# Optimization experiments

Measured on AMD Instinct MI355X. Metric: run time of the kernel, lower is better.

The kernel has to match this reference:

```python
import jax, jax.numpy as jnp
import numpy as np

EPS_KERNEL = 1e-4
EPS_DENOM = 1e-8


def setup_inputs() -> dict:
    key = jax.random.key(0)
    k1, k2, k3, k4 = jax.random.split(key, 4)
    b, h, n, d = 4, 8, 8192, 64
    nb_features = 266
    return {
        "q": jax.random.normal(k1, (b, h, n, d), dtype=jnp.float32),
        "k": jax.random.normal(k2, (b, h, n, d), dtype=jnp.float32),
        "v": jax.random.normal(k3, (b, h, n, d), dtype=jnp.float32),
        "proj": jax.random.normal(k4, (nb_features, d), dtype=jnp.float32),
    }


def _softmax_kernel(data, proj, is_query):
    # data: [b,h,n,d], proj: [f,d]
    d = data.shape[-1]
    data_normalizer = d ** (-0.25)
    ratio = proj.shape[0] ** (-0.5)
    data_dash = jnp.einsum('bhid,jd->bhij', data_normalizer * data, proj)  # [b,h,n,f]
    diag_data = (jnp.sum(data * data, axis=-1) * 0.5 * data_normalizer ** 2)[..., None]
    if is_query:
        return ratio * (jnp.exp(data_dash - diag_data
                                - jnp.max(data_dash, axis=-1, keepdims=True)) + EPS_KERNEL)
    return ratio * jnp.exp(data_dash - diag_data + EPS_KERNEL)


def reference(q, k, v, proj):
    qp = _softmax_kernel(q, proj, is_query=True)   # [b,h,n,f]
    kp = _softmax_kernel(k, proj, is_query=False)  # [b,h,n,f]
    # non-causal linear attention (never materializes the n x n matrix)
    context = jnp.einsum('bhnf,bhne->bhfe', kp, v)              # [b,h,f,e]
    d_inv = 1.0 / (jnp.einsum('bhnf,bhf->bhn', qp, kp.sum(axis=-2)) + EPS_DENOM)
    return jnp.einsum('bhfe,bhnf,bhn->bhne', context, qp, d_inv)  # [b,h,n,e]
```

## Files before the change

### kernel.cpp

```cpp
#include <hip/hip_runtime.h>
#include <hip/hip_bf16.h>
#include <math.h>


typedef __attribute__((ext_vector_type(8))) short s16x8;
typedef __attribute__((ext_vector_type(4))) float f32x4;

#define MFMA16(a,b,c) __builtin_amdgcn_mfma_f32_16x16x32_bf16((a),(b),(c),0,0,0)

__device__ __forceinline__ unsigned short bf16rne(float x){
  union { __hip_bfloat16 b; unsigned short u; } cv;
  cv.b = __float2bfloat16(x);
  return cv.u;
}
__device__ __forceinline__ float bf16tof(unsigned short h){
  return __uint_as_float(((unsigned)h) << 16);
}
__device__ __forceinline__ float exp2_fast(float x){
#if __has_builtin(__builtin_amdgcn_exp2f)
  return __builtin_amdgcn_exp2f(x);
#else
  float r; asm("v_exp_f32 %0, %1" : "=v"(r) : "v"(x)); return r;
#endif
}
__device__ __forceinline__ void cvt_hl8(const float v[8], s16x8& h, s16x8& l){
  #pragma unroll
  for(int j=0;j<8;++j){
    unsigned short hh = bf16rne(v[j]);
    h[j] = (short)hh;
    l[j] = (short)bf16rne(v[j] - bf16tof(hh));
  }
}

__global__ void fa21_prep(const float* __restrict__ proj, short* __restrict__ ph,
                          float pscale){
  int idx = blockIdx.x*256 + threadIdx.x;
  if(idx >= 288*64) return;
  int f = idx >> 6, dc = idx & 63;
  float v = (f < 266) ? proj[f*64 + dc]*pscale : 0.f;
  ph[idx] = (short)bf16rne(v);
}

__global__ __launch_bounds__(1024,1) void fa21_p1(
    const float* __restrict__ kin, const float* __restrict__ vin,
    const short* __restrict__ pjh,
    float* __restrict__ ctx_part, float* __restrict__ ksum_part,
    float koff, float diagc){
  extern __shared__ char smem[];
  char* sph = smem;
  char* skh = smem + 40960;
  float* ex = (float*)smem;
  const int tid = threadIdx.x;
  const int w = tid >> 6, lane = tid & 63, g = lane >> 4, q = lane & 15;
  const int bid = blockIdx.x;
  const int head = bid & 31, chunk = bid >> 5;
  for(int i = tid; i < 2560; i += 1024){
    int f = i >> 3;
    int byt = (f*128 + (i & 7)*16) ^ ((f & 7) << 4);
    s16x8 vh8 = {0,0,0,0,0,0,0,0};
    if(f < 288) vh8 = ((const s16x8*)pjh)[i];
    *(s16x8*)(sph + byt) = vh8;
  }
  const int mtp = w & 3, fqp = w >> 2;
  const int et  = w & 3, fqc = w >> 2;
  f32x4 acc[5];
  #pragma unroll
  for(int a=0;a<5;++a){ f32x4 z = {0.f,0.f,0.f,0.f}; acc[a] = z; }
  float ksacc[5] = {0.f,0.f,0.f,0.f,0.f};
  const float* kbase = kin + (size_t)head*8192*64;
  const float* vbase = vin + (size_t)head*8192*64;
  const float* xp  = kbase + (size_t)(chunk*1024 + mtp*16 + q)*64 + g*8;
  const float* vp  = vbase + (size_t)(chunk*1024 + 8*g)*64 + et*16 + q;
  const float* vp2 = vp + 2048;
  float4 xa0 = *(const float4*)(xp);
  float4 xb0 = *(const float4*)(xp + 4);
  float4 xa1 = *(const float4*)(xp + 32);
  float4 xb1 = *(const float4*)(xp + 36);
  __syncthreads();
  #pragma unroll 1
  for(int it = 0; it < 16; ++it){
    char* kcur = skh + (it & 1)*40960;
    s16x8 xh[2], xl[2];
    float diag;
    {
      float v0[8] = {xa0.x,xa0.y,xa0.z,xa0.w,xb0.x,xb0.y,xb0.z,xb0.w};
      float v1[8] = {xa1.x,xa1.y,xa1.z,xa1.w,xb1.x,xb1.y,xb1.z,xb1.w};
      float ss = 0.f;
      #pragma unroll
      for(int j=0;j<8;++j){ ss += v0[j]*v0[j]; ss += v1[j]*v1[j]; }
      cvt_hl8(v0, xh[0], xl[0]);
      cvt_hl8(v1, xh[1], xl[1]);
      ss += __shfl_xor(ss, 16); ss += __shfl_xor(ss, 32);
      diag = ss * diagc;
    }
    float dro[4];
    #pragma unroll
    for(int i=0;i<4;++i) dro[i] = __shfl(diag, 4*g + i) - koff;
    s16x8 vh[2], vl[2];
    {
      float vv[8];
      #pragma unroll
      for(int i2=0;i2<8;++i2) vv[i2] = vp[i2*64];
      cvt_hl8(vv, vh[0], vl[0]);
      #pragma unroll
      for(int i2=0;i2<8;++i2) vv[i2] = vp2[i2*64];
      cvt_hl8(vv, vh[1], vl[1]);
    }
    vp += 4096; vp2 += 4096;
    f32x4 S[5];
    #pragma unroll
    for(int t=0;t<5;++t){ f32x4 z = {0.f,0.f,0.f,0.f}; S[t] = z; }
    #pragma unroll
    for(int t=0; t<5; ++t){
      const int gt = fqp*5 + t;
      if(gt > 16) continue;
      const int f = gt*16 + q;
      #pragma unroll
      for(int ks=0; ks<2; ++ks){
        int byt = (f*128 + ks*64 + g*16) ^ ((f & 7) << 4);
        s16x8 bph = *(const s16x8*)(sph + byt);
        S[t] = MFMA16(xh[ks], bph, S[t]);
        S[t] = MFMA16(xl[ks], bph, S[t]);
      }
    }
    #pragma unroll
    for(int t=0; t<5; ++t){
      const int gt = fqp*5 + t;
      if(gt > 16) continue;
      const int f = gt*16 + q;
      float p[4];
      #pragma unroll
      for(int i=0;i<4;++i) p[i] = exp2_fast(S[t][i] - dro[i]);
      if(gt == 16){
        #pragma unroll
        for(int i=0;i<4;++i) p[i] = (q < 10) ? p[i] : 0.f;
      }
      ksacc[t] += p[0]+p[1]+p[2]+p[3];
      uint2 hv;
      hv.x = (unsigned)bf16rne(p[0]) | ((unsigned)bf16rne(p[1]) << 16);
      hv.y = (unsigned)bf16rne(p[2]) | ((unsigned)bf16rne(p[3]) << 16);
      int byt = (f*128 + (mtp*16 + 4*g)*2) ^ ((f & 7) << 4);
      *(uint2*)(kcur + byt) = hv;
    }
    xp += 4096;
    if(it < 15){
      xa0 = *(const float4*)(xp);
      xb0 = *(const float4*)(xp + 4);
      xa1 = *(const float4*)(xp + 32);
      xb1 = *(const float4*)(xp + 36);
    }
    __syncthreads();
    #pragma unroll
    for(int fm=0; fm<5; ++fm){
      const int gt = fqc*5 + fm;
      if(gt > 16) continue;
      const int fg = gt*16 + q;
      #pragma unroll
      for(int ks=0; ks<2; ++ks){
        int byt = (fg*128 + ks*64 + g*16) ^ ((fg & 7) << 4);
        s16x8 kf = *(const s16x8*)(kcur + byt);
        acc[fm] = MFMA16(kf, vh[ks], acc[fm]);
        acc[fm] = MFMA16(kf, vl[ks], acc[fm]);
      }
    }
  }
  {
    float* cp = ctx_part + (size_t)bid*288*64;
    #pragma unroll
    for(int fm=0; fm<5; ++fm){
      const int gt = fqc*5 + fm;
      if(gt < 18){
        #pragma unroll
        for(int i=0;i<4;++i){
          int f = gt*16 + 4*g + i;
          cp[f*64 + et*16 + q] = acc[fm][i];
        }
      }
    }
  }
  __syncthreads();
  #pragma unroll
  for(int t=0; t<5; ++t){
    float s = ksacc[t];
    s += __shfl_xor(s, 16); s += __shfl_xor(s, 32);
    if(g == 0) ex[mtp*320 + (fqp*5 + t)*16 + q] = s;
  }
  __syncthreads();
  for(int i = tid; i < 288; i += 1024)
    ksum_part[(size_t)bid*288 + i] = ex[i] + ex[320+i] + ex[640+i] + ex[960+i];
}

__global__ void fa21_reduce(const float* __restrict__ ctx_part, const float* __restrict__ ksum_part,
                            short* __restrict__ cth, float* __restrict__ ksum){
  int h = blockIdx.x >> 3, sl = blockIdx.x & 7, tid = threadIdx.x;
  for(int j = tid; j < 288*8; j += 256){
    int idx = sl*288*8 + j;
    float s = 0.f;
    #pragma unroll
    for(int c=0;c<8;++c) s += ctx_part[(size_t)(h + 32*c)*288*64 + idx];
    int f = idx >> 6, e = idx & 63;
    cth[(size_t)h*64*288 + e*288 + f] = (short)bf16rne(s);
  }
  if(sl == 0){
    for(int idx = tid; idx < 288; idx += 256){
      float s = 0.f;
      #pragma unroll
      for(int c=0;c<8;++c) s += ksum_part[(size_t)(h + 32*c)*288 + idx];
      ksum[h*288 + idx] = s;
    }
  }
}

__global__ __launch_bounds__(1024,1) void fa21_p2(
    const float* __restrict__ qin,
    const short* __restrict__ pjh,
    const short* __restrict__ cth,
    const float* __restrict__ ksum, float* __restrict__ outp,
    float qoff, float qeps, float diagc){
  extern __shared__ char smem[];
  char* sct = smem;
  char* sqp = smem + 41984;
  float* rmx = (float*)(smem + 83968);
  float* dnb = (float*)(smem + 84992);
  float* sks = (float*)(smem + 86016);
  const int tid = threadIdx.x;
  const int w = tid >> 6, lane = tid & 63, g = lane >> 4, q = lane & 15;
  const int bid = blockIdx.x;
  const int head = bid & 31, chunk = bid >> 5;
  const int mt4 = w & 3, fq = w >> 2;
  {
    const short* cb = cth + (size_t)head*18432;
    for(int i = tid; i < 2560; i += 1024){
      int e = i / 40, j = i - e*40;
      int f0 = j*8;
      s16x8 v8 = {0,0,0,0,0,0,0,0};
      if(f0 < 288) v8 = *(const s16x8*)(cb + e*288 + f0);
      *(s16x8*)(sct + e*656 + f0*2) = v8;
    }
  }
  for(int i = tid; i < 64*8; i += 1024){
    int r = i >> 3, dwi = i & 7;
    *(unsigned*)(sqp + r*656 + 544 + dwi*4) = 0u;
  }
  for(int i = tid; i < 320; i += 1024) sks[i] = (i < 288) ? ksum[head*288 + i] : 0.f;
  s16x8 aph[5][2];
  #pragma unroll
  for(int t=0; t<5; ++t){
    const int f = (fq*5 + t)*16 + q;
    #pragma unroll
    for(int ks=0; ks<2; ++ks){
      s16x8 v8 = {0,0,0,0,0,0,0,0};
      if(f < 288) v8 = *(const s16x8*)(pjh + f*64 + ks*32 + g*8);
      aph[t][ks] = v8;
    }
  }
  const float* qbase = qin + (size_t)head*8192*64;
  float* obase = outp + (size_t)head*8192*64;
  const float* xp = qbase + (size_t)(chunk*1024 + mt4*16 + q)*64 + g*8;
  float* op = obase + (size_t)(chunk*1024 + mt4*16 + 4*g)*64 + fq*16 + q;
  __syncthreads();
  #pragma unroll 1
  for(int it=0; it<16; ++it){
    s16x8 xh[2], xl[2];
    float diag;
    {
      float4 a0 = *(const float4*)(xp);
      float4 b0 = *(const float4*)(xp + 4);
      float4 a1 = *(const float4*)(xp + 32);
      float4 b1 = *(const float4*)(xp + 36);
      float v0[8] = {a0.x,a0.y,a0.z,a0.w,b0.x,b0.y,b0.z,b0.w};
      float v1[8] = {a1.x,a1.y,a1.z,a1.w,b1.x,b1.y,b1.z,b1.w};
      float ss = 0.f;
      #pragma unroll
      for(int j=0;j<8;++j){ ss += v0[j]*v0[j]; ss += v1[j]*v1[j]; }
      cvt_hl8(v0, xh[0], xl[0]);
      cvt_hl8(v1, xh[1], xl[1]);
      ss += __shfl_xor(ss, 16); ss += __shfl_xor(ss, 32);
      diag = ss * diagc;
    }
    xp += 4096;
    f32x4 S[5];
    #pragma unroll
    for(int t=0;t<5;++t){ f32x4 z = {0.f,0.f,0.f,0.f}; S[t] = z; }
    #pragma unroll
    for(int t=0; t<5; ++t){
      if(fq*5 + t > 16) continue;
      #pragma unroll
      for(int ks=0; ks<2; ++ks){
        S[t] = MFMA16(aph[t][ks], xh[ks], S[t]);
        S[t] = MFMA16(aph[t][ks], xl[ks], S[t]);
      }
    }
    float m = -3e38f;
    #pragma unroll
    for(int t=0; t<5; ++t){
      const int gt = fq*5 + t;
      if(gt > 16) continue;
      if(gt == 16){
        const int fb = gt*16 + 4*g;
        #pragma unroll
        for(int i=0;i<4;++i){
          float v = (fb + i < 266) ? S[t][i] : -3e38f;
          m = fmaxf(m, v);
        }
      } else {
        m = fmaxf(m, fmaxf(fmaxf(S[t][0], S[t][1]), fmaxf(S[t][2], S[t][3])));
      }
    }
    m = fmaxf(m, __shfl_xor(m, 16));
    m = fmaxf(m, __shfl_xor(m, 32));
    if(lane < 16) rmx[fq*64 + mt4*16 + q] = m;
    __syncthreads();
    const int nrow = mt4*16 + q;
    float rm = fmaxf(fmaxf(rmx[nrow], rmx[64 + nrow]),
                     fmaxf(rmx[128 + nrow], rmx[192 + nrow]));
    const float dro = diag + rm - qoff;
    float dnp = 0.f;
    #pragma unroll
    for(int t=0; t<5; ++t){
      const int gt = fq*5 + t;
      if(gt > 16) continue;
      const int fb = gt*16 + 4*g;
      f32x4 kv = *(const f32x4*)(sks + fb);
      float pe[4];
      #pragma unroll
      for(int i=0;i<4;++i){
        pe[i] = exp2_fast(S[t][i] - dro) + qeps;
        dnp += pe[i] * kv[i];
      }
      uint2 hv;
      hv.x = (unsigned)bf16rne(pe[0]) | ((unsigned)bf16rne(pe[1]) << 16);
      hv.y = (unsigned)bf16rne(pe[2]) | ((unsigned)bf16rne(pe[3]) << 16);
      *(uint2*)(sqp + nrow*656 + fb*2) = hv;
    }
    dnp += __shfl_xor(dnp, 16);
    dnp += __shfl_xor(dnp, 32);
    if(lane < 16) dnb[fq*64 + nrow] = dnp;
    __syncthreads();
    f32x4 dsum;
    {
      f32x4 d0 = *(const f32x4*)(dnb +       mt4*16 + 4*g);
      f32x4 d1 = *(const f32x4*)(dnb +  64 + mt4*16 + 4*g);
      f32x4 d2 = *(const f32x4*)(dnb + 128 + mt4*16 + 4*g);
      f32x4 d3 = *(const f32x4*)(dnb + 192 + mt4*16 + 4*g);
      #pragma unroll
      for(int i=0;i<4;++i) dsum[i] = d0[i] + d1[i] + d2[i] + d3[i];
    }
    f32x4 oacc = {0.f,0.f,0.f,0.f};
    #pragma unroll
    for(int ks=0; ks<9; ++ks){
      s16x8 ah = *(const s16x8*)(sqp + (mt4*16 + q)*656 + ks*64 + g*16);
      s16x8 ch = *(const s16x8*)(sct + (fq*16 + q)*656 + ks*64 + g*16);
      oacc = MFMA16(ah, ch, oacc);
    }
    #pragma unroll
    for(int i=0;i<4;++i){
      op[i*64] = oacc[i] / (dsum[i] + 1e-8f);
    }
    op += 4096;
  }
}

extern "C" void kernel_launch(void* const* d_in, const int* in_sizes, int n_in,
                              void* d_out, int out_size, void* d_ws, size_t ws_size,
                              hipStream_t stream){
  const float* q    = (const float*)d_in[0];
  const float* k    = (const float*)d_in[1];
  const float* v    = (const float*)d_in[2];
  const float* proj = (const float*)d_in[3];
  float* out = (float*)d_out;
  char* ws = (char*)d_ws;
  short* wproj_h = (short*)(ws);
  float* wctx    = (float*)(ws + 73728);
  float* wksump  = (float*)(ws + 18948096);
  short* wct_h   = (short*)(ws + 19243008);
  float* wksum   = (float*)(ws + 20422656);

  const double LOG2E = 1.4426950408889634;
  const double ln_ratio = -0.5*log(266.0);
  float pscale = (float)(pow(64.0, -0.25) * LOG2E);
  float diagc  = (float)(0.0625 * LOG2E);
  float koff   = (float)((1e-4 + ln_ratio) * LOG2E);
  float qoff   = (float)(ln_ratio * LOG2E);
  float qeps   = (float)(1e-4 / sqrt(266.0));

  hipFuncSetAttribute((const void*)fa21_p1, hipFuncAttributeMaxDynamicSharedMemorySize, 122880);
  hipFuncSetAttribute((const void*)fa21_p2, hipFuncAttributeMaxDynamicSharedMemorySize, 87296);

  fa21_prep<<<72, 256, 0, stream>>>(proj, wproj_h, pscale);
  fa21_p1<<<256, 1024, 122880, stream>>>(k, v, wproj_h, wctx, wksump, koff, diagc);
  fa21_reduce<<<256, 256, 0, stream>>>(wctx, wksump, wct_h, wksum);
  fa21_p2<<<256, 1024, 87296, stream>>>(q, wproj_h, wct_h, wksum, out,
                                        qoff, qeps, diagc);
}
```

Baseline: 174.6 us.

## Software-pipeline fa21_p2 with double-buffered qp tiles to drop one barrier per iteration

Restructures the query-side loop into a two-stage software pipeline. The qp tile, row max and denominator buffers are double-buffered in LDS, so iteration i computes features for tile i while doing the output MFMA for tile i-1, and only one __syncthreads is needed per iteration instead of two. The qp row stride shrinks from 656 to 592 bytes so both buffers fit, which raises dynamic shared memory to about 120 KB and changes LDS bank-conflict behaviour. The pipeline needs one extra drain iteration.

```diff
diff --git a/kernel.cpp b/kernel.cpp
--- a/kernel.cpp
+++ b/kernel.cpp
@@ -220,9 +220,9 @@
   extern __shared__ char smem[];
   char* sct = smem;
   char* sqp = smem + 41984;
-  float* rmx = (float*)(smem + 83968);
-  float* dnb = (float*)(smem + 84992);
-  float* sks = (float*)(smem + 86016);
+  float* rmx = (float*)(smem + 117760);
+  float* dnb = (float*)(smem + 119808);
+  float* sks = (float*)(smem + 121856);
   const int tid = threadIdx.x;
   const int w = tid >> 6, lane = tid & 63, g = lane >> 4, q = lane & 15;
   const int bid = blockIdx.x;
@@ -238,9 +238,9 @@
       *(s16x8*)(sct + e*656 + f0*2) = v8;
     }
   }
-  for(int i = tid; i < 64*8; i += 1024){
-    int r = i >> 3, dwi = i & 7;
-    *(unsigned*)(sqp + r*656 + 544 + dwi*4) = 0u;
+  for(int i = tid; i < 1024; i += 1024){
+    int b = i >> 9, r = (i >> 3) & 63, dwi = i & 7;
+    *(unsigned*)(sqp + b*37888 + r*592 + 544 + dwi*4) = 0u;
   }
   for(int i = tid; i < 320; i += 1024) sks[i] = (i < 288) ? ksum[head*288 + i] : 0.f;
   s16x8 aph[5][2];
@@ -258,106 +258,115 @@
   float* obase = outp + (size_t)head*8192*64;
   const float* xp = qbase + (size_t)(chunk*1024 + mt4*16 + q)*64 + g*8;
   float* op = obase + (size_t)(chunk*1024 + mt4*16 + 4*g)*64 + fq*16 + q;
+  const int nrow = mt4*16 + q;
   __syncthreads();
   #pragma unroll 1
-  for(int it=0; it<16; ++it){
-    s16x8 xh[2], xl[2];
-    float diag;
-    {
-      float4 a0 = *(const float4*)(xp);
-      float4 b0 = *(const float4*)(xp + 4);
-      float4 a1 = *(const float4*)(xp + 32);
-      float4 b1 = *(const float4*)(xp + 36);
-      float v0[8] = {a0.x,a0.y,a0.z,a0.w,b0.x,b0.y,b0.z,b0.w};
-      float v1[8] = {a1.x,a1.y,a1.z,a1.w,b1.x,b1.y,b1.z,b1.w};
-      float ss = 0.f;
-      #pragma unroll
-      for(int j=0;j<8;++j){ ss += v0[j]*v0[j]; ss += v1[j]*v1[j]; }
-      cvt_hl8(v0, xh[0], xl[0]);
-      cvt_hl8(v1, xh[1], xl[1]);
-      ss += __shfl_xor(ss, 16); ss += __shfl_xor(ss, 32);
-      diag = ss * diagc;
-    }
-    xp += 4096;
+  for(int it=0; it<=16; ++it){
     f32x4 S[5];
-    #pragma unroll
-    for(int t=0;t<5;++t){ f32x4 z = {0.f,0.f,0.f,0.f}; S[t] = z; }
-    #pragma unroll
-    for(int t=0; t<5; ++t){
-      if(fq*5 + t > 16) continue;
-      #pragma unroll
-      for(int ks=0; ks<2; ++ks){
-        S[t] = MFMA16(aph[t][ks], xh[ks], S[t]);
-        S[t] = MFMA16(aph[t][ks], xl[ks], S[t]);
-      }
-    }
-    float m = -3e38f;
-    #pragma unroll
-    for(int t=0; t<5; ++t){
-      const int gt = fq*5 + t;
-      if(gt > 16) continue;
-      if(gt == 16){
+    float diag = 0.f;
+    if(it < 16){
+      s16x8 xh[2], xl[2];
+      {
+        float4 a0 = *(const float4*)(xp);
+        float4 b0 = *(const float4*)(xp + 4);
+        float4 a1 = *(const float4*)(xp + 32);
+        float4 b1 = *(const float4*)(xp + 36);
+        float v0[8] = {a0.x,a0.y,a0.z,a0.w,b0.x,b0.y,b0.z,b0.w};
+        float v1[8] = {a1.x,a1.y,a1.z,a1.w,b1.x,b1.y,b1.z,b1.w};
+        float ss = 0.f;
+        #pragma unroll
+        for(int j=0;j<8;++j){ ss += v0[j]*v0[j]; ss += v1[j]*v1[j]; }
+        cvt_hl8(v0, xh[0], xl[0]);
+        cvt_hl8(v1, xh[1], xl[1]);
+        ss += __shfl_xor(ss, 16); ss += __shfl_xor(ss, 32);
+        diag = ss * diagc;
+      }
+      xp += 4096;
+      #pragma unroll
+      for(int t=0;t<5;++t){ f32x4 z = {0.f,0.f,0.f,0.f}; S[t] = z; }
+      #pragma unroll
+      for(int t=0; t<5; ++t){
+        if(fq*5 + t > 16) continue;
+        #pragma unroll
+        for(int ks=0; ks<2; ++ks){
+          S[t] = MFMA16(aph[t][ks], xh[ks], S[t]);
+          S[t] = MFMA16(aph[t][ks], xl[ks], S[t]);
+        }
+      }
+      float m = -3e38f;
+      #pragma unroll
+      for(int t=0; t<5; ++t){
+        const int gt = fq*5 + t;
+        if(gt > 16) continue;
+        if(gt == 16){
+          const int fb = gt*16 + 4*g;
+          #pragma unroll
+          for(int i=0;i<4;++i){
+            float v = (fb + i < 266) ? S[t][i] : -3e38f;
+            m = fmaxf(m, v);
+          }
+        } else {
+          m = fmaxf(m, fmaxf(fmaxf(S[t][0], S[t][1]), fmaxf(S[t][2], S[t][3])));
+        }
+      }
+      m = fmaxf(m, __shfl_xor(m, 16));
+      m = fmaxf(m, __shfl_xor(m, 32));
+      if(lane < 16) rmx[(it & 1)*256 + fq*64 + nrow] = m;
+    }
+    __syncthreads();
+    if(it < 16){
+      const int cb = (it & 1);
+      float rm = fmaxf(fmaxf(rmx[cb*256 + nrow], rmx[cb*256 + 64 + nrow]),
+                       fmaxf(rmx[cb*256 + 128 + nrow], rmx[cb*256 + 192 + nrow]));
+      const float dro = diag + rm - qoff;
+      float dnp = 0.f;
+      char* qcur = sqp + cb*37888;
+      #pragma unroll
+      for(int t=0; t<5; ++t){
+        const int gt = fq*5 + t;
+        if(gt > 16) continue;
         const int fb = gt*16 + 4*g;
+        f32x4 kv = *(const f32x4*)(sks + fb);
+        float pe[4];
         #pragma unroll
         for(int i=0;i<4;++i){
-          float v = (fb + i < 266) ? S[t][i] : -3e38f;
-          m = fmaxf(m, v);
+          pe[i] = exp2_fast(S[t][i] - dro) + qeps;
+          dnp += pe[i] * kv[i];
         }
-      } else {
-        m = fmaxf(m, fmaxf(fmaxf(S[t][0], S[t][1]), fmaxf(S[t][2], S[t][3])));
-      }
-    }
-    m = fmaxf(m, __shfl_xor(m, 16));
-    m = fmaxf(m, __shfl_xor(m, 32));
-    if(lane < 16) rmx[fq*64 + mt4*16 + q] = m;
-    __syncthreads();
-    const int nrow = mt4*16 + q;
-    float rm = fmaxf(fmaxf(rmx[nrow], rmx[64 + nrow]),
-                     fmaxf(rmx[128 + nrow], rmx[192 + nrow]));
-    const float dro = diag + rm - qoff;
-    float dnp = 0.f;
-    #pragma unroll
-    for(int t=0; t<5; ++t){
-      const int gt = fq*5 + t;
-      if(gt > 16) continue;
-      const int fb = gt*16 + 4*g;
-      f32x4 kv = *(const f32x4*)(sks + fb);
-      float pe[4];
+        uint2 hv;
+        hv.x = (unsigned)bf16rne(pe[0]) | ((unsigned)bf16rne(pe[1]) << 16);
+        hv.y = (unsigned)bf16rne(pe[2]) | ((unsigned)bf16rne(pe[3]) << 16);
+        *(uint2*)(qcur + nrow*592 + fb*2) = hv;
+      }
+      dnp += __shfl_xor(dnp, 16);
+      dnp += __shfl_xor(dnp, 32);
+      if(lane < 16) dnb[cb*256 + fq*64 + nrow] = dnp;
+    }
+    if(it > 0){
+      const int pb = ((it - 1) & 1);
+      const char* qprev = sqp + pb*37888;
+      f32x4 dsum;
+      {
+        f32x4 d0 = *(const f32x4*)(dnb + pb*256 +       mt4*16 + 4*g);
+        f32x4 d1 = *(const f32x4*)(dnb + pb*256 +  64 + mt4*16 + 4*g);
+        f32x4 d2 = *(const f32x4*)(dnb + pb*256 + 128 + mt4*16 + 4*g);
+        f32x4 d3 = *(const f32x4*)(dnb + pb*256 + 192 + mt4*16 + 4*g);
+        #pragma unroll
+        for(int i=0;i<4;++i) dsum[i] = d0[i] + d1[i] + d2[i] + d3[i];
+      }
+      f32x4 oacc = {0.f,0.f,0.f,0.f};
+      #pragma unroll
+      for(int ks=0; ks<9; ++ks){
+        s16x8 ah = *(const s16x8*)(qprev + (mt4*16 + q)*592 + ks*64 + g*16);
+        s16x8 ch = *(const s16x8*)(sct + (fq*16 + q)*656 + ks*64 + g*16);
+        oacc = MFMA16(ah, ch, oacc);
+      }
       #pragma unroll
       for(int i=0;i<4;++i){
-        pe[i] = exp2_fast(S[t][i] - dro) + qeps;
-        dnp += pe[i] * kv[i];
-      }
-      uint2 hv;
-      hv.x = (unsigned)bf16rne(pe[0]) | ((unsigned)bf16rne(pe[1]) << 16);
-      hv.y = (unsigned)bf16rne(pe[2]) | ((unsigned)bf16rne(pe[3]) << 16);
-      *(uint2*)(sqp + nrow*656 + fb*2) = hv;
-    }
-    dnp += __shfl_xor(dnp, 16);
-    dnp += __shfl_xor(dnp, 32);
-    if(lane < 16) dnb[fq*64 + nrow] = dnp;
-    __syncthreads();
-    f32x4 dsum;
-    {
-      f32x4 d0 = *(const f32x4*)(dnb +       mt4*16 + 4*g);
-      f32x4 d1 = *(const f32x4*)(dnb +  64 + mt4*16 + 4*g);
-      f32x4 d2 = *(const f32x4*)(dnb + 128 + mt4*16 + 4*g);
-      f32x4 d3 = *(const f32x4*)(dnb + 192 + mt4*16 + 4*g);
-      #pragma unroll
-      for(int i=0;i<4;++i) dsum[i] = d0[i] + d1[i] + d2[i] + d3[i];
-    }
-    f32x4 oacc = {0.f,0.f,0.f,0.f};
-    #pragma unroll
-    for(int ks=0; ks<9; ++ks){
-      s16x8 ah = *(const s16x8*)(sqp + (mt4*16 + q)*656 + ks*64 + g*16);
-      s16x8 ch = *(const s16x8*)(sct + (fq*16 + q)*656 + ks*64 + g*16);
-      oacc = MFMA16(ah, ch, oacc);
-    }
-    #pragma unroll
-    for(int i=0;i<4;++i){
-      op[i*64] = oacc[i] / (dsum[i] + 1e-8f);
-    }
-    op += 4096;
+        op[i*64] = oacc[i] / (dsum[i] + 1e-8f);
+      }
+      op += 4096;
+    }
   }
 }
 
@@ -385,11 +394,11 @@
   float qeps   = (float)(1e-4 / sqrt(266.0));
 
   hipFuncSetAttribute((const void*)fa21_p1, hipFuncAttributeMaxDynamicSharedMemorySize, 122880);
-  hipFuncSetAttribute((const void*)fa21_p2, hipFuncAttributeMaxDynamicSharedMemorySize, 87296);
+  hipFuncSetAttribute((const void*)fa21_p2, hipFuncAttributeMaxDynamicSharedMemorySize, 123136);
 
   fa21_prep<<<72, 256, 0, stream>>>(proj, wproj_h, pscale);
   fa21_p1<<<256, 1024, 122880, stream>>>(k, v, wproj_h, wctx, wksump, koff, diagc);
   fa21_reduce<<<256, 256, 0, stream>>>(wctx, wksump, wct_h, wksum);
-  fa21_p2<<<256, 1024, 87296, stream>>>(q, wproj_h, wct_h, wksum, out,
-                                        qoff, qeps, diagc);
-}
+  fa21_p2<<<256, 1024, 123136, stream>>>(q, wproj_h, wct_h, wksum, out,
+                                         qoff, qeps, diagc);
+}
```

Result: slower. 179.7 us (+2.9%).
